# Optimization experiments

Hardware: AMD Instinct MI355X
Metric: run time of the kernel (lower is better)

The kernel has to match this reference:

```python
import jax, jax.numpy as jnp
import numpy as np

N = 100000   # nodes
R = 8        # relations
E = 800000   # edges per relation
D = 128      # in_feat == out_feat
B = 4        # num bases
L = 2        # ngnn layers


def setup_inputs() -> dict:
    key = jax.random.key(0)
    ks = jax.random.split(key, 8)
    x = jax.random.normal(ks[0], (N, D), dtype=jnp.float32)
    edge_src = jax.random.randint(ks[1], (R, E), 0, N, dtype=jnp.int64)
    edge_dst = jax.random.randint(ks[2], (R, E), 0, N, dtype=jnp.int64)
    scale = 1.0 / np.sqrt(D)
    w_comp = jax.random.normal(ks[3], (R, B), dtype=jnp.float32) * 0.3
    bases = jax.random.normal(ks[4], (B, D, D), dtype=jnp.float32) * scale
    loop_weight = jax.random.normal(ks[5], (D, D), dtype=jnp.float32) * scale
    h_bias = jnp.zeros((D,), dtype=jnp.float32)
    ngnn_w = jax.random.normal(ks[6], (L, D, D), dtype=jnp.float32) * scale
    return {"x": x, "edge_src": edge_src, "edge_dst": edge_dst,
            "w_comp": w_comp, "bases": bases, "loop_weight": loop_weight,
            "h_bias": h_bias, "ngnn_w": ngnn_w}


def reference(x, edge_src, edge_dst, w_comp, bases, loop_weight, h_bias, ngnn_w):
    # basis-decomposed per-relation weights: [R, D, D]
    weight = jnp.einsum('rb,bio->rio', w_comp, bases)
    h = jnp.zeros((N, D), dtype=x.dtype)
    # per-relation GraphConv, norm='right' (mean over in-degree, clamp min 1),
    # in_feat == out_feat so DGL aggregates first then applies weight;
    # HeteroGraphConv sums relation outputs for the shared dst type.
    for r in range(R):
        src, dst = edge_src[r], edge_dst[r]
        msg = jax.ops.segment_sum(x[src], dst, num_segments=N)           # [N, D]
        deg = jax.ops.segment_sum(jnp.ones((E,), x.dtype), dst, num_segments=N)
        agg = msg / jnp.maximum(deg, 1.0)[:, None]
        h = h + agg @ weight[r]
    # self loop + bias + activation
    h = jax.nn.relu(h + x @ loop_weight + h_bias)
    # NGNN MLP (dropout is identity in eval)
    for l in range(ngnn_w.shape[0]):
        h = jax.nn.relu(h @ ngnn_w[l])
    return h
```

## Files before the change

kernel.cpp:

```cpp
#include <hip/hip_runtime.h>
#include <hip/hip_bf16.h>

#define N_NODES 100000
#define R_REL   8
#define E_EDGES 800000
#define D_FEAT  128
#define B_BASES 4
#define RN      (R_REL * N_NODES)
#define RE      (R_REL * E_EDGES)

#define NBKT    784
#define BKT_CAP 9216
#define P1_TPB  256
#define P1_EPT  32
#define P1_CHUNK (P1_TPB * P1_EPT)
#define P1_NWG  ((RE + P1_CHUNK - 1) / P1_CHUNK)

#define SUB_PER_BKT 4
#define SGRID   (NBKT * SUB_PER_BKT)
#define SUBCAP  2816

#define NXW  (N_NODES * 64)
#define NW1  (128 * 640)
#define NW2  (2 * 128 * 128)

typedef __attribute__((ext_vector_type(8))) short short8;
typedef __attribute__((ext_vector_type(4))) float floatx4;

__global__ __launch_bounds__(256) void prep_kernel(
    const float* __restrict__ x, uint* __restrict__ xb,
    const float* __restrict__ bases, const float* __restrict__ loopw,
    unsigned short* __restrict__ wT,
    const float* __restrict__ ngnn_w, unsigned short* __restrict__ wT2,
    int* __restrict__ gcursor, int do_x) {
    int idx = blockIdx.x * 256 + threadIdx.x;
    if (do_x) {
        if (idx < NXW) {
            float2 v = *(const float2*)(x + 2 * (size_t)idx);
            __hip_bfloat162 h = __float22bfloat162_rn(v);
            xb[idx] = *(uint*)&h;
            return;
        }
        idx -= NXW;
    }
    if (idx < NW1) {
        int n = idx / 640, k = idx % 640;
        float v = (k < 512) ? bases[(size_t)k * 128 + n]
                            : loopw[(size_t)(k - 512) * 128 + n];
        __hip_bfloat16 h = __float2bfloat16(v);
        wT[idx] = *(unsigned short*)&h;
        return;
    }
    idx -= NW1;
    if (idx < NW2) {
        int l = idx >> 14, rem = idx & 16383;
        int n = rem >> 7, k = rem & 127;
        float v = ngnn_w[(size_t)l * 16384 + (size_t)k * 128 + n];
        __hip_bfloat16 h = __float2bfloat16(v);
        wT2[idx] = *(unsigned short*)&h;
        return;
    }
    idx -= NW2;
    if (idx < NBKT) gcursor[idx] = idx * BKT_CAP;
}

__global__ __launch_bounds__(256) void p1_kernel(
    const int* __restrict__ src, const int* __restrict__ dst,
    int* __restrict__ gcursor, int* __restrict__ ebuf2) {
    __shared__ int hist[NBKT];
    __shared__ int cnt2[NBKT];
    __shared__ int basebkt[NBKT];
    __shared__ int lofs[NBKT];
    __shared__ int aux[256];
    __shared__ int recs[P1_CHUNK];
    __shared__ unsigned short bb[P1_CHUNK];
    int t = threadIdx.x;
    for (int i = t; i < NBKT; i += 256) { hist[i] = 0; cnt2[i] = 0; }
    __syncthreads();

    int e0 = blockIdx.x * P1_CHUNK;
    int rec[P1_EPT];
    int bkt[P1_EPT];
#pragma unroll
    for (int i = 0; i < P1_EPT; ++i) {
        int e = e0 + i * P1_TPB + t;
        if (e < RE) {
            int d = dst[e];
            int s = src[e];
            int r = e / E_EDGES;
            bkt[i] = d >> 7;
            rec[i] = s | ((d & 127) << 17) | (r << 24);
            atomicAdd(&hist[bkt[i]], 1);
        } else bkt[i] = -1;
    }
    __syncthreads();

    int k0 = t * 4;
    int c0 = (k0 + 0 < NBKT) ? hist[k0 + 0] : 0;
    int c1 = (k0 + 1 < NBKT) ? hist[k0 + 1] : 0;
    int c2 = (k0 + 2 < NBKT) ? hist[k0 + 2] : 0;
    int c3 = (k0 + 3 < NBKT) ? hist[k0 + 3] : 0;
    int s1 = c0 + c1, s2 = s1 + c2, s3 = s2 + c3;
    aux[t] = s3;
    __syncthreads();
    int vv = s3;
    for (int off = 1; off < 256; off <<= 1) {
        int yv = (t >= off) ? aux[t - off] : 0;
        __syncthreads();
        vv += yv;
        aux[t] = vv;
        __syncthreads();
    }
    int total = aux[255];
    int texcl = vv - s3;
    if (k0 + 0 < NBKT) lofs[k0 + 0] = texcl;
    if (k0 + 1 < NBKT) lofs[k0 + 1] = texcl + c0;
    if (k0 + 2 < NBKT) lofs[k0 + 2] = texcl + s1;
    if (k0 + 3 < NBKT) lofs[k0 + 3] = texcl + s2;
    __syncthreads();
    for (int i = t; i < NBKT; i += 256) {
        int hv = hist[i];
        basebkt[i] = (hv > 0) ? atomicAdd(&gcursor[i], hv) : 0;
    }
    __syncthreads();

#pragma unroll
    for (int i = 0; i < P1_EPT; ++i) {
        if (bkt[i] >= 0) {
            int p = lofs[bkt[i]] + atomicAdd(&cnt2[bkt[i]], 1);
            recs[p] = rec[i];
            bb[p] = (unsigned short)bkt[i];
        }
    }
    __syncthreads();

    for (int i = t; i < total; i += 256) {
        int b = bb[i];
        int p2 = basebkt[b] + (i - lofs[b]);
        if (p2 < (b + 1) * BKT_CAP) ebuf2[p2] = recs[i];
    }
}

template <bool XB>
__global__ __launch_bounds__(512, 8) void agg3_kernel(
    const float* __restrict__ x,
    const uint*  __restrict__ xb,
    const int*   __restrict__ gcursor,
    const int*   __restrict__ ebuf2,
    const float* __restrict__ w_comp,
    __hip_bfloat162* __restrict__ y) {
    __shared__ int raw[SUBCAP];
    __shared__ int sorted[SUBCAP];
    __shared__ int cursors[256];
    __shared__ int segbeg[256];
    __shared__ int nraw;
    const int t = threadIdx.x;
    const int bucket = blockIdx.x % NBKT;
    const int sub    = blockIdx.x / NBKT;

    int cnt = gcursor[bucket] - bucket * BKT_CAP;
    if (cnt > BKT_CAP) cnt = BKT_CAP;
    const int* brec = ebuf2 + (size_t)bucket * BKT_CAP;
    if (t < 256) cursors[t] = 0;
    if (t == 0) nraw = 0;
    __syncthreads();

    const int lane = t & 63;
    const unsigned long long lmask = (1ull << lane) - 1ull;

    for (int i0 = 0; i0 < cnt; i0 += 512) {
        int i = i0 + t;
        int rec = (i < cnt) ? brec[i] : 0;
        bool match = (i < cnt) && ((((rec >> 17) & 127) >> 5) == sub);
        unsigned long long mask = __ballot(match);
        int base = 0;
        if (lane == 0) base = atomicAdd(&nraw, (int)__popcll(mask));
        base = __shfl(base, 0);
        if (match) {
            int p = base + (int)__popcll(mask & lmask);
            if (p < SUBCAP) {
                raw[p] = rec;
                int key = ((rec >> 17) & 31) * 8 + ((rec >> 24) & 7);
                atomicAdd(&cursors[key], 1);
            }
        }
    }
    __syncthreads();
    int n = nraw; if (n > SUBCAP) n = SUBCAP;

    int deg = (t < 256) ? cursors[t] : 0;
    int* aux = sorted;
    aux[t] = deg;
    __syncthreads();
    int vv = deg;
    for (int off = 1; off < 256; off <<= 1) {
        int yv = (t >= off && t < 256) ? aux[t - off] : 0;
        __syncthreads();
        vv += yv;
        aux[t] = vv;
        __syncthreads();
    }
    if (t < 256) {
        cursors[t] = vv - deg;
        segbeg[t]  = vv - deg;
    }
    __syncthreads();

    for (int i = t; i < n; i += 512) {
        int rec = raw[i];
        int key = ((rec >> 17) & 31) * 8 + ((rec >> 24) & 7);
        int pos = atomicAdd(&cursors[key], 1);
        sorted[pos] = rec & 0x1FFFF;
    }
    __syncthreads();

    const int wid = t >> 6;
    const float* xp  = x + 2 * lane;
    const uint*  xbp = xb + lane;
    for (int nn = 0; nn < 4; ++nn) {
        int nl = wid * 4 + nn;
        int node = bucket * 128 + sub * 32 + nl;
        int key0 = nl * 8;
        float2 acc[B_BASES];
#pragma unroll
        for (int b = 0; b < B_BASES; ++b) acc[b] = make_float2(0.f, 0.f);
#pragma unroll
        for (int r = 0; r < R_REL; ++r) {
            int b0 = segbeg[key0 + r];
            int e0 = cursors[key0 + r];
            int d = e0 - b0;
            float inv = 1.0f / (float)(d > 1 ? d : 1);
            float ax = 0.f, ay = 0.f;
            int i = b0;
            if (XB) {
                for (; i + 7 < e0; i += 8) {
                    int s0 = sorted[i],     s1 = sorted[i + 1];
                    int s2 = sorted[i + 2], s3 = sorted[i + 3];
                    int s4 = sorted[i + 4], s5 = sorted[i + 5];
                    int s6 = sorted[i + 6], s7 = sorted[i + 7];
                    uint u0 = xbp[(size_t)s0 * 64];
                    uint u1 = xbp[(size_t)s1 * 64];
                    uint u2 = xbp[(size_t)s2 * 64];
                    uint u3 = xbp[(size_t)s3 * 64];
                    uint u4 = xbp[(size_t)s4 * 64];
                    uint u5 = xbp[(size_t)s5 * 64];
                    uint u6 = xbp[(size_t)s6 * 64];
                    uint u7 = xbp[(size_t)s7 * 64];
                    ax += ((__uint_as_float(u0 << 16) + __uint_as_float(u1 << 16))
                         + (__uint_as_float(u2 << 16) + __uint_as_float(u3 << 16)))
                        + ((__uint_as_float(u4 << 16) + __uint_as_float(u5 << 16))
                         + (__uint_as_float(u6 << 16) + __uint_as_float(u7 << 16)));
                    ay += ((__uint_as_float(u0 & 0xFFFF0000u) + __uint_as_float(u1 & 0xFFFF0000u))
                         + (__uint_as_float(u2 & 0xFFFF0000u) + __uint_as_float(u3 & 0xFFFF0000u)))
                        + ((__uint_as_float(u4 & 0xFFFF0000u) + __uint_as_float(u5 & 0xFFFF0000u))
                         + (__uint_as_float(u6 & 0xFFFF0000u) + __uint_as_float(u7 & 0xFFFF0000u)));
                }
            }
            for (; i + 3 < e0; i += 4) {
                int s0 = sorted[i], s1 = sorted[i + 1], s2 = sorted[i + 2], s3 = sorted[i + 3];
                if (XB) {
                    uint u0 = xbp[(size_t)s0 * 64];
                    uint u1 = xbp[(size_t)s1 * 64];
                    uint u2 = xbp[(size_t)s2 * 64];
                    uint u3 = xbp[(size_t)s3 * 64];
                    ax += (__uint_as_float(u0 << 16) + __uint_as_float(u1 << 16))
                        + (__uint_as_float(u2 << 16) + __uint_as_float(u3 << 16));
                    ay += (__uint_as_float(u0 & 0xFFFF0000u) + __uint_as_float(u1 & 0xFFFF0000u))
                        + (__uint_as_float(u2 & 0xFFFF0000u) + __uint_as_float(u3 & 0xFFFF0000u));
                } else {
                    float2 a = *(const float2*)(xp + (size_t)s0 * D_FEAT);
                    float2 b = *(const float2*)(xp + (size_t)s1 * D_FEAT);
                    float2 cc = *(const float2*)(xp + (size_t)s2 * D_FEAT);
                    float2 d2 = *(const float2*)(xp + (size_t)s3 * D_FEAT);
                    ax += (a.x + b.x) + (cc.x + d2.x);
                    ay += (a.y + b.y) + (cc.y + d2.y);
                }
            }
            for (; i < e0; ++i) {
                int s = sorted[i];
                if (XB) {
                    uint u = xbp[(size_t)s * 64];
                    ax += __uint_as_float(u << 16);
                    ay += __uint_as_float(u & 0xFFFF0000u);
                } else {
                    float2 a = *(const float2*)(xp + (size_t)s * D_FEAT);
                    ax += a.x; ay += a.y;
                }
            }
#pragma unroll
            for (int b = 0; b < B_BASES; ++b) {
                float coef = w_comp[r * B_BASES + b] * inv;
                acc[b].x = fmaf(coef, ax, acc[b].x);
                acc[b].y = fmaf(coef, ay, acc[b].y);
            }
        }
        if (node < N_NODES) {
#pragma unroll
            for (int b = 0; b < B_BASES; ++b)
                y[(size_t)node * 256 + b * 64 + lane] = __float22bfloat162_rn(acc[b]);
        }
    }
}

#define TPAD 136
template <bool XB>
__global__ __launch_bounds__(256) void fused_mlp(
    const short* __restrict__ y,
    const float* __restrict__ x,
    const uint*  __restrict__ xb,
    const unsigned short* __restrict__ wT,
    const float* __restrict__ bias,
    const unsigned short* __restrict__ wT2,
    float* __restrict__ out) {
    __shared__ short tile[4][32][TPAD];
    const int wave = threadIdx.x >> 6;
    const int lane = threadIdx.x & 63;
    const int quad = lane >> 4;
    const int l16  = lane & 15;
    const int rbase = blockIdx.x * 128 + wave * 32;
    int r0 = rbase + l16;      if (r0 >= N_NODES) r0 = N_NODES - 1;
    int r1 = rbase + 16 + l16; if (r1 >= N_NODES) r1 = N_NODES - 1;
    short (*tl)[TPAD] = tile[wave];
    const int koff = quad * 8;

    floatx4 acc0[8], acc1[8];
#pragma unroll
    for (int nt = 0; nt < 8; ++nt) {
        acc0[nt] = (floatx4){0.f, 0.f, 0.f, 0.f};
        acc1[nt] = (floatx4){0.f, 0.f, 0.f, 0.f};
    }

    const short* y0 = y + (size_t)r0 * 512;
    const short* y1 = y + (size_t)r1 * 512;
    for (int ks = 0; ks < 16; ++ks) {
        int k0 = ks * 32 + koff;
        short8 a0 = *(const short8*)(y0 + k0);
        short8 a1 = *(const short8*)(y1 + k0);
#pragma unroll
        for (int nt = 0; nt < 8; ++nt) {
            int n = nt * 16 + l16;
            short8 b = *(const short8*)((const short*)wT + (size_t)n * 640 + k0);
            acc0[nt] = __builtin_amdgcn_mfma_f32_16x16x32_bf16(a0, b, acc0[nt], 0, 0, 0);
            acc1[nt] = __builtin_amdgcn_mfma_f32_16x16x32_bf16(a1, b, acc1[nt], 0, 0, 0);
        }
    }
    if (XB) {
        const short* xb0 = (const short*)xb + (size_t)r0 * 128;
        const short* xb1 = (const short*)xb + (size_t)r1 * 128;
#pragma unroll
        for (int ks = 0; ks < 4; ++ks) {
            int kl = ks * 32 + koff;
            short8 a0 = *(const short8*)(xb0 + kl);
            short8 a1 = *(const short8*)(xb1 + kl);
#pragma unroll
            for (int nt = 0; nt < 8; ++nt) {
                int n = nt * 16 + l16;
                short8 b = *(const short8*)((const short*)wT + (size_t)n * 640 + 512 + kl);
                acc0[nt] = __builtin_amdgcn_mfma_f32_16x16x32_bf16(a0, b, acc0[nt], 0, 0, 0);
                acc1[nt] = __builtin_amdgcn_mfma_f32_16x16x32_bf16(a1, b, acc1[nt], 0, 0, 0);
            }
        }
    } else {
        const float* x0 = x + (size_t)r0 * 128;
        const float* x1 = x + (size_t)r1 * 128;
#pragma unroll
        for (int ks = 0; ks < 4; ++ks) {
            int kl = ks * 32 + koff;
            union { short8 s; uint u[4]; } ua0, ua1;
            {
                float4 fa = *(const float4*)(x0 + kl);
                float4 fb = *(const float4*)(x0 + kl + 4);
                __hip_bfloat162 h0 = __float22bfloat162_rn(make_float2(fa.x, fa.y));
                __hip_bfloat162 h1 = __float22bfloat162_rn(make_float2(fa.z, fa.w));
                __hip_bfloat162 h2 = __float22bfloat162_rn(make_float2(fb.x, fb.y));
                __hip_bfloat162 h3 = __float22bfloat162_rn(make_float2(fb.z, fb.w));
                ua0.u[0] = *(uint*)&h0; ua0.u[1] = *(uint*)&h1;
                ua0.u[2] = *(uint*)&h2; ua0.u[3] = *(uint*)&h3;
            }
            {
                float4 fa = *(const float4*)(x1 + kl);
                float4 fb = *(const float4*)(x1 + kl + 4);
                __hip_bfloat162 h0 = __float22bfloat162_rn(make_float2(fa.x, fa.y));
                __hip_bfloat162 h1 = __float22bfloat162_rn(make_float2(fa.z, fa.w));
                __hip_bfloat162 h2 = __float22bfloat162_rn(make_float2(fb.x, fb.y));
                __hip_bfloat162 h3 = __float22bfloat162_rn(make_float2(fb.z, fb.w));
                ua1.u[0] = *(uint*)&h0; ua1.u[1] = *(uint*)&h1;
                ua1.u[2] = *(uint*)&h2; ua1.u[3] = *(uint*)&h3;
            }
#pragma unroll
            for (int nt = 0; nt < 8; ++nt) {
                int n = nt * 16 + l16;
                short8 b = *(const short8*)((const short*)wT + (size_t)n * 640 + 512 + kl);
                acc0[nt] = __builtin_amdgcn_mfma_f32_16x16x32_bf16(ua0.s, b, acc0[nt], 0, 0, 0);
                acc1[nt] = __builtin_amdgcn_mfma_f32_16x16x32_bf16(ua1.s, b, acc1[nt], 0, 0, 0);
            }
        }
    }

#pragma unroll
    for (int nt = 0; nt < 8; ++nt) {
        float bs = bias[nt * 16 + l16];
#pragma unroll
        for (int i = 0; i < 4; ++i) {
            int row = quad * 4 + i;
            float v0 = fmaxf(acc0[nt][i] + bs, 0.f);
            float v1 = fmaxf(acc1[nt][i] + bs, 0.f);
            __hip_bfloat16 h0 = __float2bfloat16(v0);
            __hip_bfloat16 h1 = __float2bfloat16(v1);
            tl[row][nt * 16 + l16]      = *(short*)&h0;
            tl[16 + row][nt * 16 + l16] = *(short*)&h1;
        }
    }
    __syncthreads();

#pragma unroll
    for (int l = 0; l < 2; ++l) {
        const unsigned short* wl = wT2 + l * 16384;
        short8 af0[4], af1[4];
#pragma unroll
        for (int ks = 0; ks < 4; ++ks) {
            af0[ks] = *(const short8*)&tl[l16][ks * 32 + koff];
            af1[ks] = *(const short8*)&tl[16 + l16][ks * 32 + koff];
        }
        floatx4 ac0[8], ac1[8];
#pragma unroll
        for (int nt = 0; nt < 8; ++nt) {
            ac0[nt] = (floatx4){0.f, 0.f, 0.f, 0.f};
            ac1[nt] = (floatx4){0.f, 0.f, 0.f, 0.f};
        }
#pragma unroll
        for (int ks = 0; ks < 4; ++ks) {
            int k0 = ks * 32 + koff;
#pragma unroll
            for (int nt = 0; nt < 8; ++nt) {
                int n = nt * 16 + l16;
                short8 b = *(const short8*)((const short*)wl + (size_t)n * 128 + k0);
                ac0[nt] = __builtin_amdgcn_mfma_f32_16x16x32_bf16(af0[ks], b, ac0[nt], 0, 0, 0);
                ac1[nt] = __builtin_amdgcn_mfma_f32_16x16x32_bf16(af1[ks], b, ac1[nt], 0, 0, 0);
            }
        }
        if (l == 0) {
            __syncthreads();
#pragma unroll
            for (int nt = 0; nt < 8; ++nt)
#pragma unroll
                for (int i = 0; i < 4; ++i) {
                    int row = quad * 4 + i;
                    float v0 = fmaxf(ac0[nt][i], 0.f);
                    float v1 = fmaxf(ac1[nt][i], 0.f);
                    __hip_bfloat16 h0 = __float2bfloat16(v0);
                    __hip_bfloat16 h1 = __float2bfloat16(v1);
                    tl[row][nt * 16 + l16]      = *(short*)&h0;
                    tl[16 + row][nt * 16 + l16] = *(short*)&h1;
                }
            __syncthreads();
        } else {
#pragma unroll
            for (int nt = 0; nt < 8; ++nt) {
                int n = nt * 16 + l16;
#pragma unroll
                for (int i = 0; i < 4; ++i) {
                    int m0 = rbase + quad * 4 + i;
                    int m1 = rbase + 16 + quad * 4 + i;
                    if (m0 < N_NODES)
                        out[(size_t)m0 * D_FEAT + n] = fmaxf(ac0[nt][i], 0.f);
                    if (m1 < N_NODES)
                        out[(size_t)m1 * D_FEAT + n] = fmaxf(ac1[nt][i], 0.f);
                }
            }
        }
    }
}

extern "C" void kernel_launch(void* const* d_in, const int* in_sizes, int n_in,
                              void* d_out, int out_size, void* d_ws, size_t ws_size,
                              hipStream_t stream) {
    const float* x           = (const float*)d_in[0];
    const int*   edge_src    = (const int*)d_in[1];
    const int*   edge_dst    = (const int*)d_in[2];
    const float* w_comp      = (const float*)d_in[3];
    const float* bases       = (const float*)d_in[4];
    const float* loop_weight = (const float*)d_in[5];
    const float* h_bias      = (const float*)d_in[6];
    const float* ngnn_w      = (const float*)d_in[7];
    float* out = (float*)d_out;

    char* ws = (char*)d_ws;
    size_t off = 0;
    __hip_bfloat162* y = (__hip_bfloat162*)(ws + off);
    off += (size_t)N_NODES * 512 * 2;
    int* ebuf2 = (int*)(ws + off);
    off += (size_t)NBKT * BKT_CAP * 4;
    int* gcursor = (int*)(ws + off);
    off += 4096;
    unsigned short* wT = (unsigned short*)(ws + off);
    off += (size_t)128 * 640 * 2;
    unsigned short* wT2 = (unsigned short*)(ws + off);
    off += (size_t)2 * 128 * 128 * 2;
    uint* xb = (uint*)(ws + off);
    size_t xb_bytes = (size_t)N_NODES * 64 * 4;
    const bool use_bf16_x = (ws_size >= off + xb_bytes);

    int prep_items = (use_bf16_x ? NXW : 0) + NW1 + NW2 + NBKT;
    prep_kernel<<<(prep_items + 255) / 256, 256, 0, stream>>>(
        x, xb, bases, loop_weight, wT, ngnn_w, wT2, gcursor, use_bf16_x ? 1 : 0);

    p1_kernel<<<P1_NWG, P1_TPB, 0, stream>>>(edge_src, edge_dst, gcursor, ebuf2);

    if (use_bf16_x)
        agg3_kernel<true><<<SGRID, 512, 0, stream>>>(x, xb, gcursor, ebuf2, w_comp, y);
    else
        agg3_kernel<false><<<SGRID, 512, 0, stream>>>(x, nullptr, gcursor, ebuf2, w_comp, y);

    const int MLP_GRID = (N_NODES + 127) / 128;
    if (use_bf16_x)
        fused_mlp<true><<<MLP_GRID, 256, 0, stream>>>(
            (const short*)y, x, xb, wT, h_bias, wT2, out);
    else
        fused_mlp<false><<<MLP_GRID, 256, 0, stream>>>(
            (const short*)y, x, nullptr, wT, h_bias, wT2, out);
}
```

Before: 588.3 us.

## Vectorize x conversion and edge loads, split aggregation into two launches

```diff
diff --git a/kernel.cpp b/kernel.cpp
--- a/kernel.cpp
+++ b/kernel.cpp
@@ -18,9 +18,10 @@
 
 #define SUB_PER_BKT 4
 #define SGRID   (NBKT * SUB_PER_BKT)
+#define SGRID_H (SGRID / 2)
 #define SUBCAP  2816
 
-#define NXW  (N_NODES * 64)
+#define NXW2 (N_NODES * 32)
 #define NW1  (128 * 640)
 #define NW2  (2 * 128 * 128)
 
@@ -35,13 +36,15 @@
     int* __restrict__ gcursor, int do_x) {
     int idx = blockIdx.x * 256 + threadIdx.x;
     if (do_x) {
-        if (idx < NXW) {
-            float2 v = *(const float2*)(x + 2 * (size_t)idx);
-            __hip_bfloat162 h = __float22bfloat162_rn(v);
-            xb[idx] = *(uint*)&h;
+        if (idx < NXW2) {
+            float4 v = *(const float4*)(x + 4 * (size_t)idx);
+            __hip_bfloat162 h0 = __float22bfloat162_rn(make_float2(v.x, v.y));
+            __hip_bfloat162 h1 = __float22bfloat162_rn(make_float2(v.z, v.w));
+            uint2 o = make_uint2(*(uint*)&h0, *(uint*)&h1);
+            ((uint2*)xb)[idx] = o;
             return;
         }
-        idx -= NXW;
+        idx -= NXW2;
     }
     if (idx < NW1) {
         int n = idx / 640, k = idx % 640;
@@ -82,16 +85,25 @@
     int rec[P1_EPT];
     int bkt[P1_EPT];
 #pragma unroll
-    for (int i = 0; i < P1_EPT; ++i) {
-        int e = e0 + i * P1_TPB + t;
+    for (int j = 0; j < P1_EPT / 4; ++j) {
+        int e = e0 + j * (P1_TPB * 4) + t * 4;
         if (e < RE) {
-            int d = dst[e];
-            int s = src[e];
+            int4 d4 = *(const int4*)(dst + e);
+            int4 s4 = *(const int4*)(src + e);
             int r = e / E_EDGES;
-            bkt[i] = d >> 7;
-            rec[i] = s | ((d & 127) << 17) | (r << 24);
-            atomicAdd(&hist[bkt[i]], 1);
-        } else bkt[i] = -1;
+            int dd[4] = {d4.x, d4.y, d4.z, d4.w};
+            int ss[4] = {s4.x, s4.y, s4.z, s4.w};
+#pragma unroll
+            for (int q = 0; q < 4; ++q) {
+                int ix = j * 4 + q;
+                bkt[ix] = dd[q] >> 7;
+                rec[ix] = ss[q] | ((dd[q] & 127) << 17) | (r << 24);
+                atomicAdd(&hist[bkt[ix]], 1);
+            }
+        } else {
+#pragma unroll
+            for (int q = 0; q < 4; ++q) bkt[j * 4 + q] = -1;
+        }
     }
     __syncthreads();
 
@@ -148,15 +160,17 @@
     const int*   __restrict__ gcursor,
     const int*   __restrict__ ebuf2,
     const float* __restrict__ w_comp,
-    __hip_bfloat162* __restrict__ y) {
+    __hip_bfloat162* __restrict__ y,
+    int blk_base) {
     __shared__ int raw[SUBCAP];
     __shared__ int sorted[SUBCAP];
     __shared__ int cursors[256];
     __shared__ int segbeg[256];
     __shared__ int nraw;
     const int t = threadIdx.x;
-    const int bucket = blockIdx.x % NBKT;
-    const int sub    = blockIdx.x / NBKT;
+    const int id = blockIdx.x + blk_base;
+    const int bucket = id % NBKT;
+    const int sub    = id / NBKT;
 
     int cnt = gcursor[bucket] - bucket * BKT_CAP;
     if (cnt > BKT_CAP) cnt = BKT_CAP;
@@ -501,16 +515,19 @@
     size_t xb_bytes = (size_t)N_NODES * 64 * 4;
     const bool use_bf16_x = (ws_size >= off + xb_bytes);
 
-    int prep_items = (use_bf16_x ? NXW : 0) + NW1 + NW2 + NBKT;
+    int prep_items = (use_bf16_x ? NXW2 : 0) + NW1 + NW2 + NBKT;
     prep_kernel<<<(prep_items + 255) / 256, 256, 0, stream>>>(
         x, xb, bases, loop_weight, wT, ngnn_w, wT2, gcursor, use_bf16_x ? 1 : 0);
 
     p1_kernel<<<P1_NWG, P1_TPB, 0, stream>>>(edge_src, edge_dst, gcursor, ebuf2);
 
-    if (use_bf16_x)
-        agg3_kernel<true><<<SGRID, 512, 0, stream>>>(x, xb, gcursor, ebuf2, w_comp, y);
-    else
-        agg3_kernel<false><<<SGRID, 512, 0, stream>>>(x, nullptr, gcursor, ebuf2, w_comp, y);
+    if (use_bf16_x) {
+        agg3_kernel<true><<<SGRID_H, 512, 0, stream>>>(x, xb, gcursor, ebuf2, w_comp, y, 0);
+        agg3_kernel<true><<<SGRID_H, 512, 0, stream>>>(x, xb, gcursor, ebuf2, w_comp, y, SGRID_H);
+    } else {
+        agg3_kernel<false><<<SGRID_H, 512, 0, stream>>>(x, nullptr, gcursor, ebuf2, w_comp, y, 0);
+        agg3_kernel<false><<<SGRID_H, 512, 0, stream>>>(x, nullptr, gcursor, ebuf2, w_comp, y, SGRID_H);
+    }
 
     const int MLP_GRID = (N_NODES + 127) / 128;
     if (use_bf16_x)
```

New measurement: 579.2 us. Within noise of the previous version (-1.5%).
